# Optimization experiments

Hardware: AMD Instinct MI355X
Metric: run time of the kernel (lower is better)

The kernel has to match this reference:

```python
import jax, jax.numpy as jnp
import numpy as np

HEADS = 16  # per module init; all heads share the same weights -> identical outputs


def setup_inputs() -> dict:
    key = jax.random.key(0)
    k1, k2, k3, k4 = jax.random.split(key, 4)
    B, S, E, HD = 8, 2048, 1024, 64  # embed_size=1024, heads=16, head_dim=64
    x = jax.random.normal(k1, (B, S, E), dtype=jnp.float32)
    Wq = jax.random.normal(k2, (HD, E), dtype=jnp.float32) * (E ** -0.5)
    Wk = jax.random.normal(k3, (HD, E), dtype=jnp.float32) * (E ** -0.5)
    Wv = jax.random.normal(k4, (HD, E), dtype=jnp.float32) * (E ** -0.5)
    return {"x": x, "Wq": Wq, "Wk": Wk, "Wv": Wv}


def reference(x, Wq, Wk, Wv):
    # Linear(embed, head_dim, bias=False): y = x @ W.T
    q = jnp.einsum('bse,de->bsd', x, Wq)  # [B,S,64]
    k = jnp.einsum('bse,de->bsd', x, Wk)
    v = jnp.einsum('bse,de->bsd', x, Wv)
    # scores [b, i(query), k(key)] -- NO scaling (scaled_factor unused in source)
    scores = jnp.einsum('bij,bkj->bik', q, k)
    # nn.Softmax(dim=1): normalize over the QUERY axis (axis=1), faithful quirk
    attn = jax.nn.softmax(scores, axis=1)
    out = jnp.matmul(attn, v)  # [B,S,64]
    # Per-head loop reuses identical weights -> concat == tile across heads
    return jnp.tile(out, (1, 1, HEADS))  # [B,S,1024]
```

## Files before the change

### kernel.cpp

```cpp
#include <hip/hip_runtime.h>

#define BATCH 8
#define SEQ   2048
#define EMB   1024
#define HD    64
#define HEADS 16
#define LOG2E 1.4426950408889634f

typedef _Float16 half8 __attribute__((ext_vector_type(8)));
typedef _Float16 half4 __attribute__((ext_vector_type(4)));
typedef float    f32x4 __attribute__((ext_vector_type(4)));

__device__ __forceinline__ float fexp2(float x) {
#if __has_builtin(__builtin_amdgcn_exp2f)
    return __builtin_amdgcn_exp2f(x);
#else
    return exp2f(x);
#endif
}

__device__ __forceinline__ void dma16(void* lds_base, const void* gsrc) {
    __builtin_amdgcn_global_load_lds(
        (const __attribute__((address_space(1))) unsigned int*)gsrc,
        (__attribute__((address_space(3))) unsigned int*)lds_base, 16, 0, 0);
}
__device__ __forceinline__ void dma4(void* lds_base, const void* gsrc) {
    __builtin_amdgcn_global_load_lds(
        (const __attribute__((address_space(1))) unsigned int*)gsrc,
        (__attribute__((address_space(3))) unsigned int*)lds_base, 4, 0, 0);
}

__global__ __launch_bounds__(256) void wcvt_kernel(
    const float* __restrict__ Wq, const float* __restrict__ Wk,
    const float* __restrict__ Wv, _Float16* __restrict__ Wh)
{
    const int m = blockIdx.y;
    const float* src = (m == 0) ? Wq : (m == 1) ? Wk : Wv;
    const float scale = (m == 0) ? LOG2E : 1.0f;
    const int idx = (blockIdx.x * 256 + threadIdx.x) * 8;
    float4 f0 = *(const float4*)(src + idx);
    float4 f1 = *(const float4*)(src + idx + 4);
    half8 h;
    h[0] = (_Float16)(f0.x * scale); h[1] = (_Float16)(f0.y * scale);
    h[2] = (_Float16)(f0.z * scale); h[3] = (_Float16)(f0.w * scale);
    h[4] = (_Float16)(f1.x * scale); h[5] = (_Float16)(f1.y * scale);
    h[6] = (_Float16)(f1.z * scale); h[7] = (_Float16)(f1.w * scale);
    *(half8*)(Wh + (size_t)m * 65536 + idx) = h;
}

__global__ __launch_bounds__(512) void qkv_kernel(
    const float* __restrict__ x, const _Float16* __restrict__ Wh,
    _Float16* __restrict__ qh, _Float16* __restrict__ kh, _Float16* __restrict__ vpt)
{
    __shared__ __align__(16) char arena[65536];
    const int t = threadIdx.x, lane = t & 63, wave = t >> 6;
    const int l15 = lane & 15, quad = lane >> 4;
    const int strip = wave & 1, grp = wave >> 1;
    const int row0 = blockIdx.x * 32;

    auto issue = [&](int buf, int k0) {
        #pragma unroll
        for (int jj = 0; jj < 4; ++jj) {
            const int j = wave * 4 + jj;
            if (j < 8) {
                const int row = j * 4 + (lane >> 4);
                const int logi = (lane & 15) ^ (row & 15);
                dma16((float*)(arena + buf * 8192) + j * 256,
                      x + (size_t)(row0 + row) * EMB + k0 + logi * 4);
            } else {
                const int jw = j - 8;
                const int dd = jw * 8 + (lane >> 3);
                const int logi = (lane & 7) ^ (dd & 7);
                dma16((_Float16*)(arena + 16384 + buf * 24576) + jw * 512,
                      Wh + (size_t)(dd >> 6) * 65536 + (size_t)(dd & 63) * EMB
                         + k0 + logi * 8);
            }
        }
    };

    issue(0, 0);
    __syncthreads();

    f32x4 acc[3] = {};
    const int xrow = strip * 16 + l15;
    for (int it = 0; it < 16; ++it) {
        const int buf = it & 1;
        if (it + 1 < 16) issue(buf ^ 1, (it + 1) * 64);
        const float* xb = (const float*)(arena + buf * 8192);
        const _Float16* wb = (const _Float16*)(arena + 16384 + buf * 24576);
        half8 a[2];
        #pragma unroll
        for (int kc = 0; kc < 2; ++kc) {
            const int s0 = kc * 8 + quad * 2;
            f32x4 u0 = *(const f32x4*)(xb + xrow * 64 + ((s0    ) ^ (l15 & 15)) * 4);
            f32x4 u1 = *(const f32x4*)(xb + xrow * 64 + ((s0 + 1) ^ (l15 & 15)) * 4);
            a[kc][0] = (_Float16)u0[0]; a[kc][1] = (_Float16)u0[1];
            a[kc][2] = (_Float16)u0[2]; a[kc][3] = (_Float16)u0[3];
            a[kc][4] = (_Float16)u1[0]; a[kc][5] = (_Float16)u1[1];
            a[kc][6] = (_Float16)u1[2]; a[kc][7] = (_Float16)u1[3];
        }
        #pragma unroll
        for (int j = 0; j < 3; ++j) {
            const int dd = (grp * 3 + j) * 16 + l15;
            #pragma unroll
            for (int kc = 0; kc < 2; ++kc) {
                half8 bfr = *(const half8*)(wb + dd * 64
                              + (((kc * 4 + quad) ^ (l15 & 7)) * 8));
                acc[j] = __builtin_amdgcn_mfma_f32_16x16x32_f16(a[kc], bfr, acc[j], 0, 0, 0);
            }
        }
        __syncthreads();
    }

    #pragma unroll
    for (int j = 0; j < 3; ++j) {
        const int c = grp * 3 + j, m = c >> 2, n = c & 3;
        if (m < 2) {
            _Float16* __restrict__ dst = (m == 0) ? qh : kh;
            #pragma unroll
            for (int r = 0; r < 4; ++r)
                dst[(size_t)(row0 + strip * 16 + quad * 4 + r) * HD + n * 16 + l15] =
                    (_Float16)acc[j][r];
        } else {
            const int rg = row0 + strip * 16 + quad * 4;
            const int b = rg >> 11, s = rg & 2047;
            half4 h;
            h[0] = (_Float16)acc[j][0]; h[1] = (_Float16)acc[j][1];
            h[2] = (_Float16)acc[j][2]; h[3] = (_Float16)acc[j][3];
            *(half4*)(vpt + ((size_t)b * HD + n * 16 + l15) * SEQ + s) = h;
        }
    }
}

__global__ __launch_bounds__(256) void stats_kernel(
    const _Float16* __restrict__ qh, const _Float16* __restrict__ kh,
    float* __restrict__ l_inv)
{
    __shared__ __align__(16) char arena[16384];
    __shared__ float red[4][32];
    const int t = threadIdx.x, lane = t & 63, wave = t >> 6;
    const int l15 = lane & 15, quad = lane >> 4;
    const int b = blockIdx.y, c0 = blockIdx.x * 32;

    half8 ka[2][2];
    #pragma unroll
    for (int kt = 0; kt < 2; ++kt) {
        const _Float16* kp = kh + ((size_t)b * SEQ + c0 + kt * 16 + l15) * HD + quad * 8;
        ka[kt][0] = *(const half8*)(kp);
        ka[kt][1] = *(const half8*)(kp + 32);
    }

    auto issue = [&](int buf, int q0) {
        #pragma unroll
        for (int jj = 0; jj < 2; ++jj) {
            const int j = wave * 2 + jj;
            const int qq = j * 8 + (lane >> 3);
            const int logi = (lane & 7) ^ (qq & 7);
            dma16((_Float16*)(arena + buf * 8192) + j * 512,
                  qh + ((size_t)b * SEQ + q0 + qq) * HD + logi * 8);
        }
    };

    issue(0, 0);
    __syncthreads();

    float csum[2][4] = {};
    const int qrow = wave * 16 + l15;
    for (int it = 0; it < 32; ++it) {
        const int buf = it & 1;
        if (it + 1 < 32) issue(buf ^ 1, (it + 1) * 64);
        const _Float16* qb = (const _Float16*)(arena + buf * 8192);
        half8 bq[2];
        #pragma unroll
        for (int kc = 0; kc < 2; ++kc)
            bq[kc] = *(const half8*)(qb + qrow * 64
                        + (((kc * 4 + quad) ^ (l15 & 7)) * 8));
        f32x4 s0 = {}, s1 = {};
        s0 = __builtin_amdgcn_mfma_f32_16x16x32_f16(ka[0][0], bq[0], s0, 0, 0, 0);
        s0 = __builtin_amdgcn_mfma_f32_16x16x32_f16(ka[0][1], bq[1], s0, 0, 0, 0);
        s1 = __builtin_amdgcn_mfma_f32_16x16x32_f16(ka[1][0], bq[0], s1, 0, 0, 0);
        s1 = __builtin_amdgcn_mfma_f32_16x16x32_f16(ka[1][1], bq[1], s1, 0, 0, 0);
        #pragma unroll
        for (int r = 0; r < 4; ++r) {
            csum[0][r] += fexp2(s0[r]);
            csum[1][r] += fexp2(s1[r]);
        }
        __syncthreads();
    }
    #pragma unroll
    for (int kt = 0; kt < 2; ++kt)
        #pragma unroll
        for (int r = 0; r < 4; ++r) {
            csum[kt][r] += __shfl_xor(csum[kt][r], 1);
            csum[kt][r] += __shfl_xor(csum[kt][r], 2);
            csum[kt][r] += __shfl_xor(csum[kt][r], 4);
            csum[kt][r] += __shfl_xor(csum[kt][r], 8);
        }
    if (l15 == 0) {
        #pragma unroll
        for (int kt = 0; kt < 2; ++kt)
            #pragma unroll
            for (int r = 0; r < 4; ++r)
                red[wave][kt * 16 + quad * 4 + r] = csum[kt][r];
    }
    __syncthreads();
    if (t < 32)
        l_inv[(size_t)b * SEQ + c0 + t] =
            1.0f / (red[0][t] + red[1][t] + red[2][t] + red[3][t]);
}

__global__ __launch_bounds__(256) void out_kernel(
    const _Float16* __restrict__ qh, const _Float16* __restrict__ kh,
    const _Float16* __restrict__ vpt, const float* __restrict__ l_inv,
    float* __restrict__ out)
{
    __shared__ __align__(16) char arena[38400];
    const int t = threadIdx.x, lane = t & 63, wave = t >> 6;
    const int l15 = lane & 15, quad = lane >> 4;
    const int rw = wave & 1, kw = wave >> 1;
    const int b = blockIdx.y, r0 = blockIdx.x * 32;

    half8 aq[2];
    {
        const _Float16* qp = qh + ((size_t)b * SEQ + r0 + rw * 16 + l15) * HD + quad * 8;
        aq[0] = *(const half8*)(qp);
        aq[1] = *(const half8*)(qp + 32);
    }

    auto issue = [&](int buf, int c0) {
        #pragma unroll
        for (int jj = 0; jj < 4; ++jj) {
            if (wave < 2) {
                const int j = wave * 4 + jj;
                const int key = j * 8 + (lane >> 3);
                const int logi = (lane & 7) ^ (key & 7);
                dma16((_Float16*)(arena + buf * 8192) + j * 512,
                      kh + ((size_t)b * SEQ + c0 + key) * HD + logi * 8);
            } else {
                const int j = (wave - 2) * 4 + jj;
                const int d = j * 8 + (lane >> 3);
                const int logi = (lane & 7) ^ (d & 7);
                dma16((_Float16*)(arena + 16384 + buf * 8192) + j * 512,
                      vpt + ((size_t)b * HD + d) * SEQ + c0 + logi * 8);
            }
        }
        if (wave == 0)
            dma4((float*)(arena + 32768) + buf * 64,
                 l_inv + (size_t)b * SEQ + c0 + lane);
    };

    issue(0, 0);
    __syncthreads();

    _Float16* psb = (_Float16*)(arena + 33280) + wave * 640;
    f32x4 oacc[4] = {};
    for (int it = 0; it < 32; ++it) {
        const int buf = it & 1;
        if (it + 1 < 32) issue(buf ^ 1, (it + 1) * 64);
        const _Float16* kb = (const _Float16*)(arena + buf * 8192);
        const _Float16* vb = (const _Float16*)(arena + 16384 + buf * 8192);
        const float*    lb = (const float*)(arena + 32768) + buf * 64;

        f32x4 s[2] = {};
        float li[2];
        #pragma unroll
        for (int ct = 0; ct < 2; ++ct) {
            const int key = kw * 32 + ct * 16 + l15;
            li[ct] = lb[key];
            #pragma unroll
            for (int kc = 0; kc < 2; ++kc) {
                half8 kf = *(const half8*)(kb + key * 64
                             + (((kc * 4 + quad) ^ (l15 & 7)) * 8));
                s[ct] = __builtin_amdgcn_mfma_f32_16x16x32_f16(aq[kc], kf, s[ct], 0, 0, 0);
            }
        }
        #pragma unroll
        for (int ct = 0; ct < 2; ++ct)
            #pragma unroll
            for (int r = 0; r < 4; ++r)
                psb[(quad * 4 + r) * 40 + ct * 16 + l15] =
                    (_Float16)(fexp2(s[ct][r]) * li[ct]);
        half8 pa = *(const half8*)(psb + l15 * 40 + quad * 8);
        #pragma unroll
        for (int n = 0; n < 4; ++n) {
            const int d = n * 16 + l15;
            half8 vf = *(const half8*)(vb + d * 64
                         + (((kw * 4 + quad) ^ (l15 & 7)) * 8));
            oacc[n] = __builtin_amdgcn_mfma_f32_16x16x32_f16(pa, vf, oacc[n], 0, 0, 0);
        }
        __syncthreads();
    }

    float* red = (float*)(arena);
    float* fin = (float*)(arena + 8704);
    if (kw == 1) {
        #pragma unroll
        for (int n = 0; n < 4; ++n)
            #pragma unroll
            for (int r = 0; r < 4; ++r)
                red[(rw * 16 + quad * 4 + r) * 68 + n * 16 + l15] = oacc[n][r];
    }
    __syncthreads();
    if (kw == 0) {
        #pragma unroll
        for (int n = 0; n < 4; ++n)
            #pragma unroll
            for (int r = 0; r < 4; ++r)
                fin[(rw * 16 + quad * 4 + r) * 68 + n * 16 + l15] =
                    oacc[n][r] + red[(rw * 16 + quad * 4 + r) * 68 + n * 16 + l15];
    }
    __syncthreads();

    const int row = t >> 3, s8 = t & 7;
    float4 u0 = *(float4*)(fin + row * 68 + s8 * 8);
    float4 u1 = *(float4*)(fin + row * 68 + s8 * 8 + 4);
    size_t base = ((size_t)b * SEQ + r0 + row) * (HD * HEADS);
    #pragma unroll
    for (int h = 0; h < HEADS; ++h) {
        *(float4*)&out[base + h * HD + s8 * 8]     = u0;
        *(float4*)&out[base + h * HD + s8 * 8 + 4] = u1;
    }
}

extern "C" void kernel_launch(void* const* d_in, const int* in_sizes, int n_in,
                              void* d_out, int out_size, void* d_ws, size_t ws_size,
                              hipStream_t stream)
{
    const float* x  = (const float*)d_in[0];
    const float* Wq = (const float*)d_in[1];
    const float* Wk = (const float*)d_in[2];
    const float* Wv = (const float*)d_in[3];
    float* out = (float*)d_out;

    const size_t N = (size_t)BATCH * SEQ * HD;
    _Float16* qh  = (_Float16*)d_ws;
    _Float16* kh  = qh + N;
    _Float16* vpt = kh + N;
    _Float16* Wh  = vpt + N;
    float* l_inv  = (float*)(Wh + 196608);

    wcvt_kernel <<<dim3(32, 3), 256, 0, stream>>>(Wq, Wk, Wv, Wh);
    qkv_kernel  <<<dim3(512),   512, 0, stream>>>(x, Wh, qh, kh, vpt);
    stats_kernel<<<dim3(64, 8), 256, 0, stream>>>(qh, kh, l_inv);
    out_kernel  <<<dim3(64, 8), 256, 0, stream>>>(qh, kh, vpt, l_inv, out);
}
```

Measured before the change: 174.6 us.

## Split stats and output kernels along sequence axis and add broadcast reduction kernel

Both the column-sum stats kernel and the output kernel now split their 2048-long reduction loop into two halves via a z grid dimension, doubling the block count from 512 to 1024 for better CU occupancy. The stats kernel writes raw partial sums, and the output kernel combines the two partials with a fast reciprocal loaded directly from global memory into registers (prefetched one step ahead) instead of via LDS DMA. The output kernel writes 64-wide partial results, and a new bcast kernel sums the two halves and writes the 16-head tiled output. This costs extra global traffic for the partials and one more launch, and the hardware reciprocal is less exact than a true division.

```diff
diff --git a/kernel.cpp b/kernel.cpp
--- a/kernel.cpp
+++ b/kernel.cpp
@@ -5,6 +5,7 @@
 #define EMB   1024
 #define HD    64
 #define HEADS 16
+#define BS    (BATCH * SEQ)
 #define LOG2E 1.4426950408889634f
 
 typedef _Float16 half8 __attribute__((ext_vector_type(8)));
@@ -19,15 +20,18 @@
 #endif
 }
 
+__device__ __forceinline__ float frcp(float x) {
+#if __has_builtin(__builtin_amdgcn_rcpf)
+    return __builtin_amdgcn_rcpf(x);
+#else
+    return 1.0f / x;
+#endif
+}
+
 __device__ __forceinline__ void dma16(void* lds_base, const void* gsrc) {
     __builtin_amdgcn_global_load_lds(
         (const __attribute__((address_space(1))) unsigned int*)gsrc,
         (__attribute__((address_space(3))) unsigned int*)lds_base, 16, 0, 0);
-}
-__device__ __forceinline__ void dma4(void* lds_base, const void* gsrc) {
-    __builtin_amdgcn_global_load_lds(
-        (const __attribute__((address_space(1))) unsigned int*)gsrc,
-        (__attribute__((address_space(3))) unsigned int*)lds_base, 4, 0, 0);
 }
 
 __global__ __launch_bounds__(256) void wcvt_kernel(
@@ -134,13 +138,14 @@
 
 __global__ __launch_bounds__(256) void stats_kernel(
     const _Float16* __restrict__ qh, const _Float16* __restrict__ kh,
-    float* __restrict__ l_inv)
+    float* __restrict__ l_part)
 {
     __shared__ __align__(16) char arena[16384];
     __shared__ float red[4][32];
     const int t = threadIdx.x, lane = t & 63, wave = t >> 6;
     const int l15 = lane & 15, quad = lane >> 4;
-    const int b = blockIdx.y, c0 = blockIdx.x * 32;
+    const int b = blockIdx.y, c0 = blockIdx.x * 32, z = blockIdx.z;
+    const int qbase = z * 1024;
 
     half8 ka[2][2];
     #pragma unroll
@@ -161,14 +166,14 @@
         }
     };
 
-    issue(0, 0);
+    issue(0, qbase);
     __syncthreads();
 
     float csum[2][4] = {};
     const int qrow = wave * 16 + l15;
-    for (int it = 0; it < 32; ++it) {
+    for (int it = 0; it < 16; ++it) {
         const int buf = it & 1;
-        if (it + 1 < 32) issue(buf ^ 1, (it + 1) * 64);
+        if (it + 1 < 16) issue(buf ^ 1, qbase + (it + 1) * 64);
         const _Float16* qb = (const _Float16*)(arena + buf * 8192);
         half8 bq[2];
         #pragma unroll
@@ -205,20 +210,21 @@
     }
     __syncthreads();
     if (t < 32)
-        l_inv[(size_t)b * SEQ + c0 + t] =
-            1.0f / (red[0][t] + red[1][t] + red[2][t] + red[3][t]);
+        l_part[(size_t)z * BS + (size_t)b * SEQ + c0 + t] =
+            red[0][t] + red[1][t] + red[2][t] + red[3][t];
 }
 
 __global__ __launch_bounds__(256) void out_kernel(
     const _Float16* __restrict__ qh, const _Float16* __restrict__ kh,
-    const _Float16* __restrict__ vpt, const float* __restrict__ l_inv,
-    float* __restrict__ out)
-{
-    __shared__ __align__(16) char arena[38400];
+    const _Float16* __restrict__ vpt, const float* __restrict__ l_part,
+    float* __restrict__ opart)
+{
+    __shared__ __align__(16) char arena[37888];
     const int t = threadIdx.x, lane = t & 63, wave = t >> 6;
     const int l15 = lane & 15, quad = lane >> 4;
     const int rw = wave & 1, kw = wave >> 1;
-    const int b = blockIdx.y, r0 = blockIdx.x * 32;
+    const int b = blockIdx.y, r0 = blockIdx.x * 32, z = blockIdx.z;
+    const int kbase = z * 1024;
 
     half8 aq[2];
     {
@@ -244,29 +250,41 @@
                       vpt + ((size_t)b * HD + d) * SEQ + c0 + logi * 8);
             }
         }
-        if (wave == 0)
-            dma4((float*)(arena + 32768) + buf * 64,
-                 l_inv + (size_t)b * SEQ + c0 + lane);
     };
 
-    issue(0, 0);
-    __syncthreads();
-
-    _Float16* psb = (_Float16*)(arena + 33280) + wave * 640;
+    const float* lp = l_part + (size_t)b * SEQ;
+    float lnxt[2][2];
+    auto loadl = [&](int c0, float (&dst)[2][2]) {
+        #pragma unroll
+        for (int ct = 0; ct < 2; ++ct) {
+            const int kg = c0 + kw * 32 + ct * 16 + l15;
+            dst[ct][0] = lp[kg];
+            dst[ct][1] = lp[BS + kg];
+        }
+    };
+
+    issue(0, kbase);
+    loadl(kbase, lnxt);
+    __syncthreads();
+
+    _Float16* psb = (_Float16*)(arena + 32768) + wave * 640;
     f32x4 oacc[4] = {};
-    for (int it = 0; it < 32; ++it) {
+    for (int it = 0; it < 16; ++it) {
         const int buf = it & 1;
-        if (it + 1 < 32) issue(buf ^ 1, (it + 1) * 64);
+        float lc[2][2];
+        lc[0][0] = lnxt[0][0]; lc[0][1] = lnxt[0][1];
+        lc[1][0] = lnxt[1][0]; lc[1][1] = lnxt[1][1];
+        if (it + 1 < 16) {
+            issue(buf ^ 1, kbase + (it + 1) * 64);
+            loadl(kbase + (it + 1) * 64, lnxt);
+        }
         const _Float16* kb = (const _Float16*)(arena + buf * 8192);
         const _Float16* vb = (const _Float16*)(arena + 16384 + buf * 8192);
-        const float*    lb = (const float*)(arena + 32768) + buf * 64;
 
         f32x4 s[2] = {};
-        float li[2];
         #pragma unroll
         for (int ct = 0; ct < 2; ++ct) {
             const int key = kw * 32 + ct * 16 + l15;
-            li[ct] = lb[key];
             #pragma unroll
             for (int kc = 0; kc < 2; ++kc) {
                 half8 kf = *(const half8*)(kb + key * 64
@@ -275,11 +293,13 @@
             }
         }
         #pragma unroll
-        for (int ct = 0; ct < 2; ++ct)
+        for (int ct = 0; ct < 2; ++ct) {
+            const float li = frcp(lc[ct][0] + lc[ct][1]);
             #pragma unroll
             for (int r = 0; r < 4; ++r)
                 psb[(quad * 4 + r) * 40 + ct * 16 + l15] =
-                    (_Float16)(fexp2(s[ct][r]) * li[ct]);
+                    (_Float16)(fexp2(s[ct][r]) * li);
+        }
         half8 pa = *(const half8*)(psb + l15 * 40 + quad * 8);
         #pragma unroll
         for (int n = 0; n < 4; ++n) {
@@ -314,12 +334,25 @@
     const int row = t >> 3, s8 = t & 7;
     float4 u0 = *(float4*)(fin + row * 68 + s8 * 8);
     float4 u1 = *(float4*)(fin + row * 68 + s8 * 8 + 4);
-    size_t base = ((size_t)b * SEQ + r0 + row) * (HD * HEADS);
-    #pragma unroll
-    for (int h = 0; h < HEADS; ++h) {
-        *(float4*)&out[base + h * HD + s8 * 8]     = u0;
-        *(float4*)&out[base + h * HD + s8 * 8 + 4] = u1;
-    }
+    float* dst = opart + (size_t)z * ((size_t)BS * HD)
+               + ((size_t)b * SEQ + r0 + row) * HD + s8 * 8;
+    *(float4*)(dst)     = u0;
+    *(float4*)(dst + 4) = u1;
+}
+
+__global__ __launch_bounds__(256) void bcast_kernel(
+    const float* __restrict__ opart, float* __restrict__ out)
+{
+    const int row = blockIdx.x;
+    const int t = threadIdx.x;
+    const int d = (t * 4) & 63;
+    const float* o0 = opart + (size_t)row * HD + d;
+    const float* o1 = o0 + (size_t)BS * HD;
+    float4 a = *(const float4*)o0;
+    float4 c = *(const float4*)o1;
+    float4 s;
+    s.x = a.x + c.x; s.y = a.y + c.y; s.z = a.z + c.z; s.w = a.w + c.w;
+    *(float4*)(out + (size_t)row * (HD * HEADS) + t * 4) = s;
 }
 
 extern "C" void kernel_launch(void* const* d_in, const int* in_sizes, int n_in,
@@ -337,10 +370,12 @@
     _Float16* kh  = qh + N;
     _Float16* vpt = kh + N;
     _Float16* Wh  = vpt + N;
-    float* l_inv  = (float*)(Wh + 196608);
-
-    wcvt_kernel <<<dim3(32, 3), 256, 0, stream>>>(Wq, Wk, Wv, Wh);
-    qkv_kernel  <<<dim3(512),   512, 0, stream>>>(x, Wh, qh, kh, vpt);
-    stats_kernel<<<dim3(64, 8), 256, 0, stream>>>(qh, kh, l_inv);
-    out_kernel  <<<dim3(64, 8), 256, 0, stream>>>(qh, kh, vpt, l_inv, out);
-}
+    float* l_part = (float*)(Wh + 196608);
+    float* opart  = l_part + 2 * BS;
+
+    wcvt_kernel <<<dim3(32, 3),    256, 0, stream>>>(Wq, Wk, Wv, Wh);
+    qkv_kernel  <<<dim3(512),      512, 0, stream>>>(x, Wh, qh, kh, vpt);
+    stats_kernel<<<dim3(64, 8, 2), 256, 0, stream>>>(qh, kh, l_part);
+    out_kernel  <<<dim3(64, 8, 2), 256, 0, stream>>>(qh, kh, vpt, l_part, opart);
+    bcast_kernel<<<dim3(BS),       256, 0, stream>>>(opart, out);
+}
```

After: 170.0 us. 1.03x faster.
